# Kernel tuning notes

Hardware: AMD Instinct MI355X
Metric: run time of the kernel (lower is better)

Reference implementation:

```python
import jax, jax.numpy as jnp
import numpy as np

EMBED_DIM = 256
NUM_CLASSES = 10


def setup_inputs() -> dict:
    key = jax.random.key(0)
    k1, k2, k3, k4 = jax.random.split(key, 4)
    x = jax.random.normal(k1, (64, 196, 768), dtype=jnp.float32)
    ag_w = jax.random.normal(k2, (EMBED_DIM, 768), dtype=jnp.float32)
    ag_b = jax.random.normal(k3, (EMBED_DIM,), dtype=jnp.float32)
    lm_w = jax.random.normal(k4, (EMBED_DIM * NUM_CLASSES, 768), dtype=jnp.float32)
    return {"x": x, "ag_w": ag_w, "ag_b": ag_b, "lm_w": lm_w}


def reference(x, ag_w, ag_b, lm_w):
    # x: (B, HW, D); ag_w: (E, D); ag_b: (E,); lm_w: (E*C, D)
    B, HW, D = x.shape
    E, C = EMBED_DIM, NUM_CLASSES
    # frozen arrangement generator -> binary sign pattern (B, HW, E)
    sign_patterns = (jnp.einsum('bhd,ed->bhe', x, ag_w) + ag_b > 0).astype(x.dtype)
    # linear map: (B, HW, E*C) -> (B, HW, E, C)
    z = jnp.einsum('bhd,pd->bhp', x, lm_w).reshape(B, HW, E, C)
    # masked reduction over HW and embed dims
    preds = jnp.einsum('bhp,bhpc->bc', sign_patterns, z) / HW
    return preds / E
```

## Files before the change

### kernel.cpp

```cpp
#include <hip/hip_runtime.h>

#define B_    64
#define HW_   196
#define HWP_  224
#define D_    768
#define E_    256
#define C_    10
#define MP_   (B_*HWP_)
#define K3K_  (E_*D_)
#define K3NB_ 192

typedef __bf16 bf16x8 __attribute__((ext_vector_type(8)));
typedef __bf16 bf16x4 __attribute__((ext_vector_type(4)));
typedef float  f32x4  __attribute__((ext_vector_type(4)));

__device__ __forceinline__ void gld_lds16(const void* g, void* l) {
  __builtin_amdgcn_global_load_lds((const __attribute__((address_space(1))) void*)g,
                                   (__attribute__((address_space(3))) void*)l, 16, 0, 0);
}

__global__ __launch_bounds__(256) void k0_x(const float* __restrict__ x,
                                            __bf16* __restrict__ xhi,
                                            __bf16* __restrict__ xlo) {
  size_t i4 = ((size_t)blockIdx.x * 256 + threadIdx.x) * 4;
  int d  = (int)(i4 % D_);
  size_t row = i4 / D_;
  int hp = (int)(row % HWP_);
  int b  = (int)(row / HWP_);
  float4 v = make_float4(0.f, 0.f, 0.f, 0.f);
  if (hp < HW_) v = *(const float4*)&x[((size_t)b * HW_ + hp) * D_ + d];
  float vv[4] = {v.x, v.y, v.z, v.w};
  bf16x4 h, l;
#pragma unroll
  for (int j = 0; j < 4; j++) {
    __bf16 hj = (__bf16)vv[j];
    float r = vv[j] - (float)hj;
    h[j] = hj;
    l[j] = (__bf16)r;
  }
  *(bf16x4*)&xhi[i4] = h;
  *(bf16x4*)&xlo[i4] = l;
}

__global__ __launch_bounds__(256) void k0_prep(const float* __restrict__ w,
                                               __bf16* __restrict__ whi,
                                               __bf16* __restrict__ wlo,
                                               const float* __restrict__ lmw,
                                               __bf16* __restrict__ w2) {
  int bid = blockIdx.x;
  if (bid < 192) {
    size_t i4 = ((size_t)bid * 256 + threadIdx.x) * 4;
    float4 v = *(const float4*)&w[i4];
    float vv[4] = {v.x, v.y, v.z, v.w};
    bf16x4 h, l;
#pragma unroll
    for (int j = 0; j < 4; j++) {
      __bf16 hj = (__bf16)vv[j];
      float r = vv[j] - (float)hj;
      h[j] = hj;
      l[j] = (__bf16)r;
    }
    *(bf16x4*)&whi[i4] = h;
    *(bf16x4*)&wlo[i4] = l;
  } else {
    size_t i4 = ((size_t)(bid - 192) * 256 + threadIdx.x) * 4;
    int c = (int)(i4 / K3K_);
    int rem = (int)(i4 - (size_t)c * K3K_);
    int e = rem / D_;
    int d = rem - e * D_;
    bf16x4 o;
    if (c < C_) {
      float4 v = *(const float4*)&lmw[((size_t)e * C_ + c) * D_ + d];
      o[0] = (__bf16)v.x; o[1] = (__bf16)v.y; o[2] = (__bf16)v.z; o[3] = (__bf16)v.w;
    } else {
      o[0] = o[1] = o[2] = o[3] = (__bf16)0.0f;
    }
    *(bf16x4*)&w2[i4] = o;
  }
}

__global__ __launch_bounds__(256) void k1_signs(const __bf16* __restrict__ xhi,
                                                const __bf16* __restrict__ xlo,
                                                const __bf16* __restrict__ whi,
                                                const __bf16* __restrict__ wlo,
                                                const float* __restrict__ bias,
                                                __bf16* __restrict__ st) {
  __shared__ __align__(16) __bf16 Ah[64 * 32];
  __shared__ __align__(16) __bf16 Al[64 * 32];
  __shared__ __align__(16) __bf16 Bh[64 * 32];
  __shared__ __align__(16) __bf16 Bl[64 * 32];
  const int m0 = blockIdx.x * 64;
  const int n0 = blockIdx.y * 64;
  const int tid = threadIdx.x;
  const int wave = tid >> 6, lane = tid & 63;
  const int wm = (wave & 1) * 32, wn = (wave >> 1) * 32;
  const int q = lane >> 4, l15 = lane & 15;
  const int sr = tid >> 2;
  const int sk = (tid & 3) * 8;
  const int ldsoff = wave * 512;
  f32x4 acc[2][2] = {};

  for (int k0 = 0; k0 < D_; k0 += 32) {
    __syncthreads();
    gld_lds16(&xhi[(size_t)(m0 + sr) * D_ + k0 + sk], &Ah[ldsoff]);
    gld_lds16(&xlo[(size_t)(m0 + sr) * D_ + k0 + sk], &Al[ldsoff]);
    gld_lds16(&whi[(size_t)(n0 + sr) * D_ + k0 + sk], &Bh[ldsoff]);
    gld_lds16(&wlo[(size_t)(n0 + sr) * D_ + k0 + sk], &Bl[ldsoff]);
    __syncthreads();
    bf16x8 af[2], alf[2], bfh[2], bfl[2];
#pragma unroll
    for (int t = 0; t < 2; t++) {
      af[t]  = *(const bf16x8*)&Ah[(wm + t * 16 + l15) * 32 + q * 8];
      alf[t] = *(const bf16x8*)&Al[(wm + t * 16 + l15) * 32 + q * 8];
      bfh[t] = *(const bf16x8*)&Bh[(wn + t * 16 + l15) * 32 + q * 8];
      bfl[t] = *(const bf16x8*)&Bl[(wn + t * 16 + l15) * 32 + q * 8];
    }
#pragma unroll
    for (int mt = 0; mt < 2; mt++)
#pragma unroll
      for (int nt = 0; nt < 2; nt++) {
        acc[mt][nt] = __builtin_amdgcn_mfma_f32_16x16x32_bf16(af[mt],  bfh[nt], acc[mt][nt], 0, 0, 0);
        acc[mt][nt] = __builtin_amdgcn_mfma_f32_16x16x32_bf16(alf[mt], bfh[nt], acc[mt][nt], 0, 0, 0);
        acc[mt][nt] = __builtin_amdgcn_mfma_f32_16x16x32_bf16(af[mt],  bfl[nt], acc[mt][nt], 0, 0, 0);
      }
  }
#pragma unroll
  for (int mt = 0; mt < 2; mt++)
#pragma unroll
    for (int nt = 0; nt < 2; nt++) {
      int e = n0 + wn + nt * 16 + l15;
      float bv = bias[e];
#pragma unroll
      for (int r = 0; r < 4; r++) {
        int m = m0 + wm + mt * 16 + q * 4 + r;
        int b = m / HWP_;
        int hp = m - b * HWP_;
        float v = acc[mt][nt][r] + bv;
        __bf16 s = (hp < HW_ && v > 0.0f) ? (__bf16)1.0f : (__bf16)0.0f;
        st[((size_t)b * E_ + e) * HWP_ + hp] = s;
      }
    }
}

__global__ __launch_bounds__(256) void k2_g(const __bf16* __restrict__ st,
                                            const __bf16* __restrict__ xhi,
                                            __bf16* __restrict__ g) {
  __shared__ __align__(16) __bf16 As[128 * 32];
  __shared__ __align__(16) __bf16 Bs[128 * 40];
  const int b  = blockIdx.y;
  const int e0 = (blockIdx.x / 6) * 128;
  const int d0 = (blockIdx.x % 6) * 128;
  const int tid = threadIdx.x;
  const int wave = tid >> 6, lane = tid & 63;
  const int wm = (wave & 1) * 64, wn = (wave >> 1) * 64;
  const int q = lane >> 4, l15 = lane & 15;
  const int sr = tid >> 2, sk = (tid & 3) * 8;
  const int ldsoff = wave * 512;
  const int kk4 = ((tid >> 2) & 7) * 4;
  const int dgroup = (tid & 3) | (((tid >> 5) & 7) << 2);
  const int dc0 = dgroup * 4;
  f32x4 acc[4][4] = {};

  for (int k0 = 0; k0 < HWP_; k0 += 32) {
    __syncthreads();
    gld_lds16(&st[((size_t)b * E_ + e0 + sr) * HWP_ + k0 + sk],      &As[ldsoff]);
    gld_lds16(&st[((size_t)b * E_ + e0 + 64 + sr) * HWP_ + k0 + sk], &As[64 * 32 + ldsoff]);
    {
      const __bf16* src = &xhi[((size_t)b * HWP_ + k0 + kk4) * D_ + d0 + dc0];
      bf16x4 r0 = *(const bf16x4*)&src[0];
      bf16x4 r1 = *(const bf16x4*)&src[D_];
      bf16x4 r2 = *(const bf16x4*)&src[2 * D_];
      bf16x4 r3 = *(const bf16x4*)&src[3 * D_];
#pragma unroll
      for (int j = 0; j < 4; j++) {
        bf16x4 o;
        o[0] = r0[j]; o[1] = r1[j]; o[2] = r2[j]; o[3] = r3[j];
        *(bf16x4*)&Bs[(dc0 + j) * 40 + kk4] = o;
      }
    }
    __syncthreads();
    bf16x8 af[4], bfr[4];
#pragma unroll
    for (int t = 0; t < 4; t++) {
      af[t]  = *(const bf16x8*)&As[(wm + t * 16 + l15) * 32 + q * 8];
      bfr[t] = *(const bf16x8*)&Bs[(wn + t * 16 + l15) * 40 + q * 8];
    }
#pragma unroll
    for (int mt = 0; mt < 4; mt++)
#pragma unroll
      for (int nt = 0; nt < 4; nt++)
        acc[mt][nt] = __builtin_amdgcn_mfma_f32_16x16x32_bf16(af[mt], bfr[nt], acc[mt][nt], 0, 0, 0);
  }
#pragma unroll
  for (int mt = 0; mt < 4; mt++)
#pragma unroll
    for (int nt = 0; nt < 4; nt++) {
      int d = d0 + wn + nt * 16 + l15;
#pragma unroll
      for (int r = 0; r < 4; r++) {
        int e = e0 + wm + mt * 16 + q * 4 + r;
        g[((size_t)b * E_ + e) * D_ + d] = (__bf16)acc[mt][nt][r];
      }
    }
}

__global__ __launch_bounds__(256) void k3_mfma(const __bf16* __restrict__ g,
                                               const __bf16* __restrict__ w2,
                                               float* __restrict__ out) {
  __shared__ float sp[B_ * C_];
  const int tid = threadIdx.x;
  const int wave = tid >> 6, lane = tid & 63;
  const int q = lane >> 4, l15 = lane & 15;
  const int kbase = blockIdx.x * (K3K_ / K3NB_) + wave * 256;
  f32x4 acc[4] = {};

  for (int i = tid; i < B_ * C_; i += 256) sp[i] = 0.0f;

#pragma unroll
  for (int ks = 0; ks < 8; ks++) {
    int k = kbase + ks * 32 + q * 8;
    bf16x8 bfrag = *(const bf16x8*)&w2[(size_t)l15 * K3K_ + k];
#pragma unroll
    for (int mt = 0; mt < 4; mt++) {
      bf16x8 afrag = *(const bf16x8*)&g[(size_t)(mt * 16 + l15) * K3K_ + k];
      acc[mt] = __builtin_amdgcn_mfma_f32_16x16x32_bf16(afrag, bfrag, acc[mt], 0, 0, 0);
    }
  }
  __syncthreads();
  int c = l15;
  if (c < C_) {
#pragma unroll
    for (int mt = 0; mt < 4; mt++)
#pragma unroll
      for (int r = 0; r < 4; r++) {
        int b = mt * 16 + q * 4 + r;
        atomicAdd(&sp[b * C_ + c], acc[mt][r]);
      }
  }
  __syncthreads();
  const float scale = 1.0f / (196.0f * 256.0f);
  for (int i = tid; i < B_ * C_; i += 256) atomicAdd(&out[i], sp[i] * scale);
}

extern "C" void kernel_launch(void* const* d_in, const int* in_sizes, int n_in,
                              void* d_out, int out_size, void* d_ws, size_t ws_size,
                              hipStream_t stream) {
  const float* x    = (const float*)d_in[0];
  const float* ag_w = (const float*)d_in[1];
  const float* ag_b = (const float*)d_in[2];
  const float* lm_w = (const float*)d_in[3];
  float* out = (float*)d_out;

  char* ws = (char*)d_ws;
  const size_t XP_BYTES = (size_t)B_ * HWP_ * D_ * 2;
  const size_t W_BYTES  = (size_t)E_ * D_ * 2;
  const size_t ST_BYTES = (size_t)B_ * E_ * HWP_ * 2;
  const size_t G_BYTES  = (size_t)B_ * E_ * D_ * 2;
  __bf16* xhi = (__bf16*)(ws);
  __bf16* xlo = (__bf16*)(ws + XP_BYTES);
  __bf16* whi = (__bf16*)(ws + 2 * XP_BYTES);
  __bf16* wlo = (__bf16*)(ws + 2 * XP_BYTES + W_BYTES);
  __bf16* st  = (__bf16*)(ws + 2 * XP_BYTES + 2 * W_BYTES);
  __bf16* gb  = (__bf16*)(ws + 2 * XP_BYTES + 2 * W_BYTES + ST_BYTES);
  __bf16* w2  = (__bf16*)(ws + 2 * XP_BYTES + 2 * W_BYTES + ST_BYTES + G_BYTES);

  hipMemsetAsync(d_out, 0, (size_t)out_size * sizeof(float), stream);

  k0_x<<<dim3((B_ * HWP_ * D_) / 4 / 256), dim3(256), 0, stream>>>(x, xhi, xlo);
  k0_prep<<<dim3(192 + (16 * K3K_) / 4 / 256), dim3(256), 0, stream>>>(ag_w, whi, wlo, lm_w, w2);
  k1_signs<<<dim3(MP_ / 64, E_ / 64), dim3(256), 0, stream>>>(xhi, xlo, whi, wlo, ag_b, st);
  k2_g<<<dim3((E_ / 128) * (D_ / 128), B_), dim3(256), 0, stream>>>(st, xhi, gb);
  k3_mfma<<<dim3(K3NB_), dim3(256), 0, stream>>>(gb, w2, out);
}
```

Before: 164.2 us.

## Double-buffer LDS tiles in sign and G GEMM kernels to overlap loads

Adds ping-pong LDS buffers to k1_signs and k2_g. Each iteration issues the global loads for the next K tile (async global_load_lds, plus register loads for the transposed xhi tile) before running the MFMAs on the current tile, and only stores the transposed tile afterward. This is meant to hide global memory latency behind compute and cut one barrier per iteration. In exchange it doubles LDS use, which may lower occupancy, and it relies on the single remaining barrier to also cover completion of the async LDS loads.

```diff
diff --git a/kernel.cpp b/kernel.cpp
--- a/kernel.cpp
+++ b/kernel.cpp
@@ -85,10 +85,10 @@
                                                 const __bf16* __restrict__ wlo,
                                                 const float* __restrict__ bias,
                                                 __bf16* __restrict__ st) {
-  __shared__ __align__(16) __bf16 Ah[64 * 32];
-  __shared__ __align__(16) __bf16 Al[64 * 32];
-  __shared__ __align__(16) __bf16 Bh[64 * 32];
-  __shared__ __align__(16) __bf16 Bl[64 * 32];
+  __shared__ __align__(16) __bf16 Ah[2][64 * 32];
+  __shared__ __align__(16) __bf16 Al[2][64 * 32];
+  __shared__ __align__(16) __bf16 Bh[2][64 * 32];
+  __shared__ __align__(16) __bf16 Bl[2][64 * 32];
   const int m0 = blockIdx.x * 64;
   const int n0 = blockIdx.y * 64;
   const int tid = threadIdx.x;
@@ -100,20 +100,32 @@
   const int ldsoff = wave * 512;
   f32x4 acc[2][2] = {};
 
+  const __bf16* gAh = &xhi[(size_t)(m0 + sr) * D_ + sk];
+  const __bf16* gAl = &xlo[(size_t)(m0 + sr) * D_ + sk];
+  const __bf16* gBh = &whi[(size_t)(n0 + sr) * D_ + sk];
+  const __bf16* gBl = &wlo[(size_t)(n0 + sr) * D_ + sk];
+
+  gld_lds16(gAh, &Ah[0][ldsoff]);
+  gld_lds16(gAl, &Al[0][ldsoff]);
+  gld_lds16(gBh, &Bh[0][ldsoff]);
+  gld_lds16(gBl, &Bl[0][ldsoff]);
+  __syncthreads();
+
+  int cur = 0;
   for (int k0 = 0; k0 < D_; k0 += 32) {
-    __syncthreads();
-    gld_lds16(&xhi[(size_t)(m0 + sr) * D_ + k0 + sk], &Ah[ldsoff]);
-    gld_lds16(&xlo[(size_t)(m0 + sr) * D_ + k0 + sk], &Al[ldsoff]);
-    gld_lds16(&whi[(size_t)(n0 + sr) * D_ + k0 + sk], &Bh[ldsoff]);
-    gld_lds16(&wlo[(size_t)(n0 + sr) * D_ + k0 + sk], &Bl[ldsoff]);
-    __syncthreads();
+    if (k0 + 32 < D_) {
+      gld_lds16(gAh + k0 + 32, &Ah[cur ^ 1][ldsoff]);
+      gld_lds16(gAl + k0 + 32, &Al[cur ^ 1][ldsoff]);
+      gld_lds16(gBh + k0 + 32, &Bh[cur ^ 1][ldsoff]);
+      gld_lds16(gBl + k0 + 32, &Bl[cur ^ 1][ldsoff]);
+    }
     bf16x8 af[2], alf[2], bfh[2], bfl[2];
 #pragma unroll
     for (int t = 0; t < 2; t++) {
-      af[t]  = *(const bf16x8*)&Ah[(wm + t * 16 + l15) * 32 + q * 8];
-      alf[t] = *(const bf16x8*)&Al[(wm + t * 16 + l15) * 32 + q * 8];
-      bfh[t] = *(const bf16x8*)&Bh[(wn + t * 16 + l15) * 32 + q * 8];
-      bfl[t] = *(const bf16x8*)&Bl[(wn + t * 16 + l15) * 32 + q * 8];
+      af[t]  = *(const bf16x8*)&Ah[cur][(wm + t * 16 + l15) * 32 + q * 8];
+      alf[t] = *(const bf16x8*)&Al[cur][(wm + t * 16 + l15) * 32 + q * 8];
+      bfh[t] = *(const bf16x8*)&Bh[cur][(wn + t * 16 + l15) * 32 + q * 8];
+      bfl[t] = *(const bf16x8*)&Bl[cur][(wn + t * 16 + l15) * 32 + q * 8];
     }
 #pragma unroll
     for (int mt = 0; mt < 2; mt++)
@@ -123,6 +135,8 @@
         acc[mt][nt] = __builtin_amdgcn_mfma_f32_16x16x32_bf16(alf[mt], bfh[nt], acc[mt][nt], 0, 0, 0);
         acc[mt][nt] = __builtin_amdgcn_mfma_f32_16x16x32_bf16(af[mt],  bfl[nt], acc[mt][nt], 0, 0, 0);
       }
+    __syncthreads();
+    cur ^= 1;
   }
 #pragma unroll
   for (int mt = 0; mt < 2; mt++)
@@ -145,8 +159,8 @@
 __global__ __launch_bounds__(256) void k2_g(const __bf16* __restrict__ st,
                                             const __bf16* __restrict__ xhi,
                                             __bf16* __restrict__ g) {
-  __shared__ __align__(16) __bf16 As[128 * 32];
-  __shared__ __align__(16) __bf16 Bs[128 * 40];
+  __shared__ __align__(16) __bf16 As[2][128 * 32];
+  __shared__ __align__(16) __bf16 Bs[2][128 * 40];
   const int b  = blockIdx.y;
   const int e0 = (blockIdx.x / 6) * 128;
   const int d0 = (blockIdx.x % 6) * 128;
@@ -161,35 +175,60 @@
   const int dc0 = dgroup * 4;
   f32x4 acc[4][4] = {};
 
+  const __bf16* gA0 = &st[((size_t)b * E_ + e0 + sr) * HWP_ + sk];
+  const __bf16* gA1 = &st[((size_t)b * E_ + e0 + 64 + sr) * HWP_ + sk];
+  const __bf16* gB  = &xhi[((size_t)b * HWP_ + kk4) * D_ + d0 + dc0];
+
+  gld_lds16(gA0, &As[0][ldsoff]);
+  gld_lds16(gA1, &As[0][64 * 32 + ldsoff]);
+  {
+    bf16x4 r0 = *(const bf16x4*)&gB[0];
+    bf16x4 r1 = *(const bf16x4*)&gB[D_];
+    bf16x4 r2 = *(const bf16x4*)&gB[2 * D_];
+    bf16x4 r3 = *(const bf16x4*)&gB[3 * D_];
+#pragma unroll
+    for (int j = 0; j < 4; j++) {
+      bf16x4 o;
+      o[0] = r0[j]; o[1] = r1[j]; o[2] = r2[j]; o[3] = r3[j];
+      *(bf16x4*)&Bs[0][(dc0 + j) * 40 + kk4] = o;
+    }
+  }
+  __syncthreads();
+
+  int cur = 0;
   for (int k0 = 0; k0 < HWP_; k0 += 32) {
-    __syncthreads();
-    gld_lds16(&st[((size_t)b * E_ + e0 + sr) * HWP_ + k0 + sk],      &As[ldsoff]);
-    gld_lds16(&st[((size_t)b * E_ + e0 + 64 + sr) * HWP_ + k0 + sk], &As[64 * 32 + ldsoff]);
-    {
-      const __bf16* src = &xhi[((size_t)b * HWP_ + k0 + kk4) * D_ + d0 + dc0];
-      bf16x4 r0 = *(const bf16x4*)&src[0];
-      bf16x4 r1 = *(const bf16x4*)&src[D_];
-      bf16x4 r2 = *(const bf16x4*)&src[2 * D_];
-      bf16x4 r3 = *(const bf16x4*)&src[3 * D_];
+    const bool have = (k0 + 32 < HWP_);
+    bf16x4 r0, r1, r2, r3;
+    if (have) {
+      gld_lds16(gA0 + k0 + 32, &As[cur ^ 1][ldsoff]);
+      gld_lds16(gA1 + k0 + 32, &As[cur ^ 1][64 * 32 + ldsoff]);
+      const __bf16* src = gB + (size_t)(k0 + 32) * D_;
+      r0 = *(const bf16x4*)&src[0];
+      r1 = *(const bf16x4*)&src[D_];
+      r2 = *(const bf16x4*)&src[2 * D_];
+      r3 = *(const bf16x4*)&src[3 * D_];
+    }
+    bf16x8 af[4], bfr[4];
+#pragma unroll
+    for (int t = 0; t < 4; t++) {
+      af[t]  = *(const bf16x8*)&As[cur][(wm + t * 16 + l15) * 32 + q * 8];
+      bfr[t] = *(const bf16x8*)&Bs[cur][(wn + t * 16 + l15) * 40 + q * 8];
+    }
+#pragma unroll
+    for (int mt = 0; mt < 4; mt++)
+#pragma unroll
+      for (int nt = 0; nt < 4; nt++)
+        acc[mt][nt] = __builtin_amdgcn_mfma_f32_16x16x32_bf16(af[mt], bfr[nt], acc[mt][nt], 0, 0, 0);
+    if (have) {
 #pragma unroll
       for (int j = 0; j < 4; j++) {
         bf16x4 o;
         o[0] = r0[j]; o[1] = r1[j]; o[2] = r2[j]; o[3] = r3[j];
-        *(bf16x4*)&Bs[(dc0 + j) * 40 + kk4] = o;
+        *(bf16x4*)&Bs[cur ^ 1][(dc0 + j) * 40 + kk4] = o;
       }
     }
     __syncthreads();
-    bf16x8 af[4], bfr[4];
-#pragma unroll
-    for (int t = 0; t < 4; t++) {
-      af[t]  = *(const bf16x8*)&As[(wm + t * 16 + l15) * 32 + q * 8];
-      bfr[t] = *(const bf16x8*)&Bs[(wn + t * 16 + l15) * 40 + q * 8];
-    }
-#pragma unroll
-    for (int mt = 0; mt < 4; mt++)
-#pragma unroll
-      for (int nt = 0; nt < 4; nt++)
-        acc[mt][nt] = __builtin_amdgcn_mfma_f32_16x16x32_bf16(af[mt], bfr[nt], acc[mt][nt], 0, 0, 0);
+    cur ^= 1;
   }
 #pragma unroll
   for (int mt = 0; mt < 4; mt++)
```

Result: no change. 163.3 us (-0.5%).
